# Performance work log

Measured on AMD Instinct MI355X. Metric: run time of the kernel, lower is better.

Reference implementation:

```python
import jax, jax.numpy as jnp
import numpy as np

B, S, D, K = 8, 2048, 1024, 256
LN_EPS = 1e-5


def _freq_positions(input_dim, num_freq, spec_len):
    # torch.linspace(0, input_dim//2, num_freq).long(), clamped to rfft length
    pos = np.linspace(0.0, input_dim // 2, num_freq).astype(np.int64)
    return np.clip(pos, 0, spec_len - 1)


def setup_inputs() -> dict:
    key = jax.random.key(0)
    k1, k2, k3 = jax.random.split(key, 3)
    x = jax.random.normal(k1, (B, S, D), dtype=jnp.float32)
    # magnitude init: init_magnitude=0.1 (small jitter keeps gradients non-degenerate)
    magnitude = 0.1 + 0.01 * jax.random.normal(k2, (K, D), dtype=jnp.float32)
    phase = 0.1 * jax.random.normal(k3, (K, D), dtype=jnp.float32)
    interference_w = 0.01 * jax.random.normal(jax.random.fold_in(key, 7), (K, K), dtype=jnp.float32)
    ln_gamma = jnp.ones((D,), dtype=jnp.float32)
    ln_beta = jnp.zeros((D,), dtype=jnp.float32)
    return {"x": x, "magnitude": magnitude, "phase": phase,
            "interference_w": interference_w, "ln_gamma": ln_gamma, "ln_beta": ln_beta}


def reference(x, magnitude, phase, interference_w, ln_gamma, ln_beta):
    b, s, d = x.shape
    residual = x
    padded_len = 1 << int(np.ceil(np.log2(s)))  # static
    if padded_len > s:
        x = jnp.pad(x, ((0, 0), (0, padded_len - s), (0, 0)))
    # FFT along sequence axis: (B, padded_len//2+1, D) complex
    x_fft = jnp.fft.rfft(x, axis=1)
    freq_pos = _freq_positions(d, magnitude.shape[0], x_fft.shape[1])  # (K,) static ints

    # gather selected frequencies: (B, K, D)
    x_selected = x_fft[:, freq_pos, :]
    # complex weights from magnitude/phase
    cw = (magnitude * jnp.cos(phase) + 1j * magnitude * jnp.sin(phase)).astype(jnp.complex64)
    x_weighted = x_selected * cw[None, :, :]
    # interference on real part: bkd,kj->bjd
    interference = jnp.einsum('bkd,kj->bjd', jnp.real(x_weighted), interference_w)
    x_processed = x_weighted + 0.1 * interference.astype(jnp.complex64)

    # scatter back (positions are unique for these dims)
    x_fft_processed = x_fft.at[:, freq_pos, :].set(x_processed)
    x_rec = jnp.fft.irfft(x_fft_processed, n=padded_len, axis=1)[:, :s, :]

    # residual + LayerNorm over last dim (dropout is identity in eval)
    y = x_rec + residual
    mu = jnp.mean(y, axis=-1, keepdims=True)
    var = jnp.mean(jnp.square(y - mu), axis=-1, keepdims=True)
    y = (y - mu) * jax.lax.rsqrt(var + LN_EPS)
    return y * ln_gamma + ln_beta
```

## Files before the change

### kernel.cpp

```cpp
#include <hip/hip_runtime.h>
#include <math.h>

#define NS 2048
#define ND 1024
#define NK 256
#define NB 8

typedef __attribute__((ext_vector_type(8))) short short8;
typedef __attribute__((ext_vector_type(4))) float f32x4;
typedef __attribute__((ext_vector_type(4))) unsigned short u16x4;
typedef __attribute__((ext_vector_type(8))) unsigned short u16x8;
typedef unsigned int u32;

__device__ __forceinline__ unsigned short f2bf(float x) {
  unsigned int u = __float_as_uint(x);
  u = (u + 0x7fffu + ((u >> 16) & 1u)) >> 16;
  return (unsigned short)u;
}
__device__ __forceinline__ float bf2f(unsigned short h) {
  return __uint_as_float(((unsigned int)h) << 16);
}

__device__ __forceinline__ int fpos(int k) {
  return (k == 255) ? 512 : (int)((float)k * (512.0f / 255.0f));
}

__device__ __forceinline__ void gll16(const unsigned short* g, unsigned short* l) {
  __builtin_amdgcn_global_load_lds(
      (__attribute__((address_space(1))) void*)(void*)const_cast<unsigned short*>(g),
      (__attribute__((address_space(3))) void*)l, 16, 0, 0);
}

__global__ __launch_bounds__(256) void k_master(float* __restrict__ master) {
  int t = blockIdx.x * 256 + threadIdx.x;
  double th = (double)t * (6.283185307179586476925286766559 / 2048.0);
  master[t] = (float)cos(th);
}

__global__ __launch_bounds__(256) void k_tabs(const float* __restrict__ master,
                                              unsigned short* __restrict__ CFi,
                                              unsigned short* __restrict__ CSi) {
  int gid = blockIdx.x * 256 + threadIdx.x;
  if (gid < 512 * 2048) {
    int r = gid >> 11, s = gid & 2047;
    int p = (fpos(r >> 1) * s) & 2047;
    float v = (r & 1) ? -master[(p + 1536) & 2047] : master[p];
    CFi[gid] = f2bf(v);
  } else {
    int g = gid - 512 * 2048;
    int s = g >> 9, c = g & 511;
    int p = (fpos(c >> 1) * s) & 2047;
    float v = (c & 1) ? -master[(p + 1536) & 2047] : master[p];
    CSi[g] = f2bf(v);
  }
}

__global__ __launch_bounds__(256) void k_cw2(const float* __restrict__ mag,
                                             const float* __restrict__ ph,
                                             float* __restrict__ mc,
                                             float* __restrict__ ms,
                                             float* __restrict__ mcT,
                                             float* __restrict__ msT) {
  int bid = blockIdx.x;
  int kt = bid >> 4, dt = bid & 15;
  int t = threadIdx.x;
  __shared__ float lc[64][68], ls[64][68];
  int kl = t >> 4, d4 = (t & 15) * 4;
#pragma unroll
  for (int i = 0; i < 4; i++) {
    int k = i * 16 + kl;
    size_t off = (size_t)(kt * 64 + k) * ND + dt * 64 + d4;
    float4 mg = *(const float4*)&mag[off];
    float4 pp = *(const float4*)&ph[off];
    float m[4] = {mg.x, mg.y, mg.z, mg.w}, p[4] = {pp.x, pp.y, pp.z, pp.w};
    float oc[4], os[4];
#pragma unroll
    for (int q = 0; q < 4; q++) {
      float sp, cp;
      sincosf(p[q], &sp, &cp);
      oc[q] = m[q] * cp;
      os[q] = m[q] * sp;
      lc[k][d4 + q] = oc[q];
      ls[k][d4 + q] = os[q];
    }
    *(float4*)&mc[off] = make_float4(oc[0], oc[1], oc[2], oc[3]);
    *(float4*)&ms[off] = make_float4(os[0], os[1], os[2], os[3]);
  }
  __syncthreads();
  int dl = t >> 2, kc = (t & 3) * 16;
#pragma unroll
  for (int i = 0; i < 16; i += 4) {
    float4 vc = {lc[kc + i][dl], lc[kc + i + 1][dl], lc[kc + i + 2][dl], lc[kc + i + 3][dl]};
    float4 vs = {ls[kc + i][dl], ls[kc + i + 1][dl], ls[kc + i + 2][dl], ls[kc + i + 3][dl]};
    size_t o = (size_t)(dt * 64 + dl) * 256 + kt * 64 + kc + i;
    *(float4*)&mcT[o] = vc;
    *(float4*)&msT[o] = vs;
  }
}

__global__ __launch_bounds__(256) void k_wt(const float* __restrict__ W,
                                            unsigned short* __restrict__ WT) {
  int bid = blockIdx.x;
  int kt = bid >> 2, jt = bid & 3;
  int t = threadIdx.x;
  __shared__ float lw[64][68];
  int kl = t >> 4, j4 = (t & 15) * 4;
#pragma unroll
  for (int i = 0; i < 4; i++) {
    int k = i * 16 + kl;
    float4 wv = *(const float4*)&W[(size_t)(kt * 64 + k) * 256 + jt * 64 + j4];
    lw[k][j4 + 0] = wv.x; lw[k][j4 + 1] = wv.y;
    lw[k][j4 + 2] = wv.z; lw[k][j4 + 3] = wv.w;
  }
  __syncthreads();
  int jl = t >> 2, kc = (t & 3) * 16;
#pragma unroll
  for (int i = 0; i < 16; i += 4) {
    u16x4 v = {f2bf(lw[kc + i][jl]), f2bf(lw[kc + i + 1][jl]),
               f2bf(lw[kc + i + 2][jl]), f2bf(lw[kc + i + 3][jl])};
    *(u16x4*)&WT[(size_t)(jt * 64 + jl) * 256 + kt * 64 + kc + i] = v;
  }
}

__global__ __launch_bounds__(256) void k_conv(const float* __restrict__ x,
                                              unsigned short* __restrict__ xt) {
  int bid = blockIdx.x;
  int b = bid >> 9, rem = bid & 511;
  int s0 = (rem >> 4) * 64, d0 = (rem & 15) * 64;
  int t = threadIdx.x;
  __shared__ __attribute__((aligned(16))) unsigned short lt[64 * 72];
#pragma unroll
  for (int c = 0; c < 4; c++) {
    int e = c * 256 + t;
    int row = e >> 4, col = (e & 15) * 4;
    float4 v = *(const float4*)&x[((size_t)b * NS + s0 + row) * ND + d0 + col];
    lt[(col + 0) * 72 + row] = f2bf(v.x);
    lt[(col + 1) * 72 + row] = f2bf(v.y);
    lt[(col + 2) * 72 + row] = f2bf(v.z);
    lt[(col + 3) * 72 + row] = f2bf(v.w);
  }
  __syncthreads();
  int dl = t >> 2, sc = (t & 3) * 16;
  u16x8 a = *(u16x8*)&lt[dl * 72 + sc];
  u16x8 bb = *(u16x8*)&lt[dl * 72 + sc + 8];
  size_t o = ((size_t)b * ND + d0 + dl) * NS + s0 + sc;
  *(u16x8*)&xt[o] = a;
  *(u16x8*)&xt[o + 8] = bb;
}

template <int BM, int BN, int EPI>
__global__ __launch_bounds__(256) void gemm_db(const unsigned short* __restrict__ A,
                                               const unsigned short* __restrict__ B,
                                               unsigned short* __restrict__ C0,
                                               unsigned short* __restrict__ C1,
                                               const float* __restrict__ P0,
                                               const float* __restrict__ P1,
                                               int M, int N, int K,
                                               size_t sA, size_t sB) {
  constexpr int MI = BM / 32, NI = BN / 32;
  constexpr int NSTG = (BM + BN) / 32;
  const int mt = M / BM, nt = N / BN;
  int nwg = gridDim.x;
  int bid0 = blockIdx.x;
  int bid = (bid0 & 7) * (nwg >> 3) + (bid0 >> 3);
  int b = bid / (mt * nt), r = bid % (mt * nt);
  int m0 = (r / nt) * BM, n0 = (r % nt) * BN;
  int t = threadIdx.x, lane = t & 63, w = t >> 6;
  int wr = (t >> 7) & 1, wc = (t >> 6) & 1;
  __shared__ __attribute__((aligned(16))) unsigned short As[2][BM * 64];
  __shared__ __attribute__((aligned(16))) unsigned short Bs[2][BN * 64];
  const unsigned short* Ag = A + b * sA + (size_t)m0 * K;
  const unsigned short* Bg = B + b * sB + (size_t)n0 * K;
  int arow = lane >> 3;
  int aswz = ((lane & 7) ^ (lane >> 3)) * 8;

  f32x4 acc[MI][NI];
#pragma unroll
  for (int i = 0; i < MI; i++)
#pragma unroll
    for (int j = 0; j < NI; j++) acc[i][j] = {0.f, 0.f, 0.f, 0.f};

  const int nkt = K / 64;

#define STAGE(buf, kt_)                                                       \
  do {                                                                        \
    int kofs = (kt_) * 64;                                                    \
    _Pragma("unroll") for (int i = 0; i < BM / 32; i++) {                     \
      int r0 = w * (BM / 4) + i * 8;                                          \
      gll16(Ag + (size_t)(r0 + arow) * K + kofs + aswz, &As[buf][r0 * 64]);   \
    }                                                                         \
    _Pragma("unroll") for (int i = 0; i < BN / 32; i++) {                     \
      int r0 = w * (BN / 4) + i * 8;                                          \
      gll16(Bg + (size_t)(r0 + arow) * K + kofs + aswz, &Bs[buf][r0 * 64]);   \
    }                                                                         \
  } while (0)

  STAGE(0, 0);
  if (nkt > 1) STAGE(1, 1);

  for (int kt = 0; kt < nkt; kt++) {
    int cur = kt & 1;
    if (kt + 1 < nkt)
      asm volatile("s_waitcnt vmcnt(%0)" ::"n"(NSTG) : "memory");
    else
      asm volatile("s_waitcnt vmcnt(0)" ::: "memory");
    __builtin_amdgcn_s_barrier();
#pragma unroll
    for (int ks = 0; ks < 2; ks++) {
      short8 af[MI], bfv[NI];
#pragma unroll
      for (int mi = 0; mi < MI; mi++) {
        int row = wr * (BM / 2) + mi * 16 + (lane & 15);
        int sl = (ks * 4 + (lane >> 4)) ^ (row & 7);
        af[mi] = *(const short8*)&As[cur][row * 64 + sl * 8];
      }
#pragma unroll
      for (int ni = 0; ni < NI; ni++) {
        int row = wc * (BN / 2) + ni * 16 + (lane & 15);
        int sl = (ks * 4 + (lane >> 4)) ^ (row & 7);
        bfv[ni] = *(const short8*)&Bs[cur][row * 64 + sl * 8];
      }
#pragma unroll
      for (int mi = 0; mi < MI; mi++)
#pragma unroll
        for (int ni = 0; ni < NI; ni++)
          acc[mi][ni] = __builtin_amdgcn_mfma_f32_16x16x32_bf16(
              af[mi], bfv[ni], acc[mi][ni], 0, 0, 0);
    }
    __builtin_amdgcn_s_barrier();
    if (kt + 2 < nkt) STAGE(cur, kt + 2);
  }
#undef STAGE

#pragma unroll
  for (int mi = 0; mi < MI; mi++) {
#pragma unroll
    for (int ni = 0; ni < NI; ni++) {
      int row0 = m0 + wr * (BM / 2) + mi * 16 + ((lane >> 4) * 4);
      int col = n0 + wc * (BN / 2) + ni * 16 + (lane & 15);
      f32x4 a = acc[mi][ni];
      if (EPI == 0) {
#pragma unroll
        for (int q = 0; q < 4; q++)
          C0[((size_t)b * M + row0 + q) * N + col] = f2bf(a[q]);
      } else if (EPI == 1) {
        u16x4 xv = {f2bf(a[0]), f2bf(a[1]), f2bf(a[2]), f2bf(a[3])};
        *(u16x4*)&C0[((size_t)b * N + col) * M + row0] = xv;
        int j0 = row0 >> 1, j1 = j0 + 1;
        float rw0 = P0[(size_t)j0 * ND + col] * a[0] - P1[(size_t)j0 * ND + col] * a[1];
        float rw1 = P0[(size_t)j1 * ND + col] * a[2] - P1[(size_t)j1 * ND + col] * a[3];
        u32 pk = (u32)f2bf(rw0) | ((u32)f2bf(rw1) << 16);
        *(u32*)&C1[((size_t)b * N + col) * (M / 2) + j0] = pk;
      } else {
        float alpha = ((col == 0) ? 1.0f : 2.0f) * (1.0f / 2048.0f);
#pragma unroll
        for (int q = 0; q < 4; q++) {
          int dd = row0 + q;
          u32 reim = *(const u32*)&C1[((size_t)b * M + dd) * 512 + 2 * col];
          float xr = bf2f((unsigned short)(reim & 0xffffu));
          float xi = bf2f((unsigned short)(reim >> 16));
          float mcv = P0[(size_t)dd * 256 + col];
          float msv = P1[(size_t)dd * 256 + col];
          float m1 = mcv - 1.0f;
          float dre = alpha * (m1 * xr - msv * xi + 0.1f * a[q]);
          float dim = alpha * (msv * xr + m1 * xi);
          u32 pk = (u32)f2bf(dre) | ((u32)f2bf(dim) << 16);
          *(u32*)&C0[((size_t)b * M + dd) * 512 + 2 * col] = pk;
        }
      }
    }
  }
}

__global__ __launch_bounds__(256) void k4_ln(const float* __restrict__ x,
                                             const unsigned short* __restrict__ corr,
                                             const float* __restrict__ g,
                                             const float* __restrict__ be,
                                             float* __restrict__ out) {
  int row = blockIdx.x;
  int t = threadIdx.x;
  size_t base = (size_t)row * ND + t * 4;
  u16x4 cv = *(const u16x4*)&corr[base];
  float4 xv = *(const float4*)&x[base];
  float v[4] = {fmaf(2.f, xv.x, bf2f(cv[0])), fmaf(2.f, xv.y, bf2f(cv[1])),
                fmaf(2.f, xv.z, bf2f(cv[2])), fmaf(2.f, xv.w, bf2f(cv[3]))};
  float s = v[0] + v[1] + v[2] + v[3];
  float q = v[0] * v[0] + v[1] * v[1] + v[2] * v[2] + v[3] * v[3];
#pragma unroll
  for (int o = 32; o >= 1; o >>= 1) {
    s += __shfl_xor(s, o, 64);
    q += __shfl_xor(q, o, 64);
  }
  __shared__ float ss[4], qs[4];
  if ((t & 63) == 0) { ss[t >> 6] = s; qs[t >> 6] = q; }
  __syncthreads();
  s = ss[0] + ss[1] + ss[2] + ss[3];
  q = qs[0] + qs[1] + qs[2] + qs[3];
  float mu = s * (1.0f / (float)ND);
  float var = q * (1.0f / (float)ND) - mu * mu;
  float rstd = rsqrtf(var + 1e-5f);
  float4 gv = *(const float4*)&g[t * 4];
  float4 bv = *(const float4*)&be[t * 4];
  float4 ov;
  ov.x = (v[0] - mu) * rstd * gv.x + bv.x;
  ov.y = (v[1] - mu) * rstd * gv.y + bv.y;
  ov.z = (v[2] - mu) * rstd * gv.z + bv.z;
  ov.w = (v[3] - mu) * rstd * gv.w + bv.w;
  *(float4*)&out[base] = ov;
}

extern "C" void kernel_launch(void* const* d_in, const int* in_sizes, int n_in,
                              void* d_out, int out_size, void* d_ws, size_t ws_size,
                              hipStream_t stream) {
  const float* x   = (const float*)d_in[0];
  const float* mag = (const float*)d_in[1];
  const float* ph  = (const float*)d_in[2];
  const float* W   = (const float*)d_in[3];
  const float* g   = (const float*)d_in[4];
  const float* be  = (const float*)d_in[5];
  float* out = (float*)d_out;
  char* w = (char*)d_ws;

  float*          master = (float*)(w);
  unsigned short* CFi    = (unsigned short*)(w + (1ull << 20));
  unsigned short* CSi    = (unsigned short*)(w + (3ull << 20));
  float*          mc     = (float*)(w + (5ull << 20));
  float*          ms     = (float*)(w + (6ull << 20));
  float*          mcT    = (float*)(w + (7ull << 20));
  float*          msT    = (float*)(w + (8ull << 20));
  unsigned short* WT     = (unsigned short*)(w + (9ull << 20));
  unsigned short* XqT    = (unsigned short*)(w + (10ull << 20));
  unsigned short* RXwT   = (unsigned short*)(w + (18ull << 20));
  unsigned short* DltT   = (unsigned short*)(w + (22ull << 20));
  unsigned short* corr   = (unsigned short*)(w + (30ull << 20));
  unsigned short* xt     = (unsigned short*)(w + (62ull << 20));

  k_master<<<8, 256, 0, stream>>>(master);
  k_tabs<<<8192, 256, 0, stream>>>(master, CFi, CSi);
  k_cw2<<<64, 256, 0, stream>>>(mag, ph, mc, ms, mcT, msT);
  k_wt<<<16, 256, 0, stream>>>(W, WT);
  k_conv<<<4096, 256, 0, stream>>>(x, xt);
  gemm_db<128, 64, 1><<<512, 256, 0, stream>>>(CFi, xt, XqT, RXwT, mc, ms,
                                               512, 1024, 2048, 0,
                                               (size_t)1024 * 2048);
  gemm_db<128, 64, 2><<<256, 256, 0, stream>>>(RXwT, WT, DltT, XqT, mcT, msT,
                                               1024, 256, 256,
                                               (size_t)1024 * 256, 0);
  gemm_db<128, 128, 0><<<1024, 256, 0, stream>>>(CSi, DltT, corr, nullptr,
                                                 nullptr, nullptr,
                                                 2048, 1024, 512, 0,
                                                 (size_t)1024 * 512);
  k4_ln<<<16384, 256, 0, stream>>>(x, corr, g, be, out);
}
```

Before: 225.3 us.

## Fuse prep kernels, load GEMM A operand from global, triple-buffer B, row-per-wave LN

Merges the master-cosine, table, complex-weight, weight-transpose and x-transpose kernels into one launch, and computes the twiddles with sincosf directly instead of through a lookup table. The GEMM now reads the A operand straight from global memory into registers and keeps only B in LDS with three buffers. This halves LDS use and moves the next-stage prefetch ahead of the MFMAs, but the A loads are uncoalesced and unswizzled. The LayerNorm kernel gives one row to each wave, which removes the shared-memory reduction and the block sync.

```diff
diff --git a/kernel.cpp b/kernel.cpp
--- a/kernel.cpp
+++ b/kernel.cpp
@@ -31,125 +31,120 @@
       (__attribute__((address_space(3))) void*)l, 16, 0, 0);
 }
 
-__global__ __launch_bounds__(256) void k_master(float* __restrict__ master) {
-  int t = blockIdx.x * 256 + threadIdx.x;
-  double th = (double)t * (6.283185307179586476925286766559 / 2048.0);
-  master[t] = (float)cos(th);
-}
-
-__global__ __launch_bounds__(256) void k_tabs(const float* __restrict__ master,
+__global__ __launch_bounds__(256) void k_prep(const float* __restrict__ mag,
+                                              const float* __restrict__ ph,
+                                              const float* __restrict__ W,
+                                              const float* __restrict__ x,
                                               unsigned short* __restrict__ CFi,
-                                              unsigned short* __restrict__ CSi) {
-  int gid = blockIdx.x * 256 + threadIdx.x;
-  if (gid < 512 * 2048) {
-    int r = gid >> 11, s = gid & 2047;
-    int p = (fpos(r >> 1) * s) & 2047;
-    float v = (r & 1) ? -master[(p + 1536) & 2047] : master[p];
-    CFi[gid] = f2bf(v);
+                                              unsigned short* __restrict__ CSi,
+                                              float* __restrict__ mc,
+                                              float* __restrict__ ms,
+                                              float* __restrict__ mcT,
+                                              float* __restrict__ msT,
+                                              unsigned short* __restrict__ WT,
+                                              unsigned short* __restrict__ xt) {
+  __shared__ __attribute__((aligned(16))) char smem[34816];
+  int bid = blockIdx.x, t = threadIdx.x;
+  const float C2PI = 0.0030679615757712823f;
+  if (bid < 8192) {
+    int gid = bid * 256 + t;
+    if (gid < 512 * 2048) {
+      int r = gid >> 11, s = gid & 2047;
+      int p = (fpos(r >> 1) * s) & 2047;
+      float sn, cs;
+      sincosf((float)p * C2PI, &sn, &cs);
+      CFi[gid] = f2bf((r & 1) ? -sn : cs);
+    } else {
+      int g2 = gid - 512 * 2048;
+      int s = g2 >> 9, c = g2 & 511;
+      int p = (fpos(c >> 1) * s) & 2047;
+      float sn, cs;
+      sincosf((float)p * C2PI, &sn, &cs);
+      CSi[g2] = f2bf((c & 1) ? -sn : cs);
+    }
+  } else if (bid < 8256) {
+    int lb = bid - 8192;
+    int kt = lb >> 4, dt = lb & 15;
+    float(*lc)[68] = (float(*)[68])smem;
+    float(*ls)[68] = (float(*)[68])(smem + 17408);
+    int kl = t >> 4, d4 = (t & 15) * 4;
+#pragma unroll
+    for (int i = 0; i < 4; i++) {
+      int k = i * 16 + kl;
+      size_t off = (size_t)(kt * 64 + k) * ND + dt * 64 + d4;
+      float4 mg = *(const float4*)&mag[off];
+      float4 pp = *(const float4*)&ph[off];
+      float m[4] = {mg.x, mg.y, mg.z, mg.w}, p[4] = {pp.x, pp.y, pp.z, pp.w};
+      float oc[4], os[4];
+#pragma unroll
+      for (int q = 0; q < 4; q++) {
+        float sp, cp;
+        sincosf(p[q], &sp, &cp);
+        oc[q] = m[q] * cp;
+        os[q] = m[q] * sp;
+        lc[k][d4 + q] = oc[q];
+        ls[k][d4 + q] = os[q];
+      }
+      *(float4*)&mc[off] = make_float4(oc[0], oc[1], oc[2], oc[3]);
+      *(float4*)&ms[off] = make_float4(os[0], os[1], os[2], os[3]);
+    }
+    __syncthreads();
+    int dl = t >> 2, kc = (t & 3) * 16;
+#pragma unroll
+    for (int i = 0; i < 16; i += 4) {
+      float4 vc = {lc[kc + i][dl], lc[kc + i + 1][dl], lc[kc + i + 2][dl], lc[kc + i + 3][dl]};
+      float4 vs = {ls[kc + i][dl], ls[kc + i + 1][dl], ls[kc + i + 2][dl], ls[kc + i + 3][dl]};
+      size_t o = (size_t)(dt * 64 + dl) * 256 + kt * 64 + kc + i;
+      *(float4*)&mcT[o] = vc;
+      *(float4*)&msT[o] = vs;
+    }
+  } else if (bid < 8272) {
+    int lb = bid - 8256;
+    int kt = lb >> 2, jt = lb & 3;
+    float(*lw)[68] = (float(*)[68])smem;
+    int kl = t >> 4, j4 = (t & 15) * 4;
+#pragma unroll
+    for (int i = 0; i < 4; i++) {
+      int k = i * 16 + kl;
+      float4 wv = *(const float4*)&W[(size_t)(kt * 64 + k) * 256 + jt * 64 + j4];
+      lw[k][j4 + 0] = wv.x; lw[k][j4 + 1] = wv.y;
+      lw[k][j4 + 2] = wv.z; lw[k][j4 + 3] = wv.w;
+    }
+    __syncthreads();
+    int jl = t >> 2, kc = (t & 3) * 16;
+#pragma unroll
+    for (int i = 0; i < 16; i += 4) {
+      u16x4 v = {f2bf(lw[kc + i][jl]), f2bf(lw[kc + i + 1][jl]),
+                 f2bf(lw[kc + i + 2][jl]), f2bf(lw[kc + i + 3][jl])};
+      *(u16x4*)&WT[(size_t)(jt * 64 + jl) * 256 + kt * 64 + kc + i] = v;
+    }
   } else {
-    int g = gid - 512 * 2048;
-    int s = g >> 9, c = g & 511;
-    int p = (fpos(c >> 1) * s) & 2047;
-    float v = (c & 1) ? -master[(p + 1536) & 2047] : master[p];
-    CSi[g] = f2bf(v);
-  }
-}
-
-__global__ __launch_bounds__(256) void k_cw2(const float* __restrict__ mag,
-                                             const float* __restrict__ ph,
-                                             float* __restrict__ mc,
-                                             float* __restrict__ ms,
-                                             float* __restrict__ mcT,
-                                             float* __restrict__ msT) {
-  int bid = blockIdx.x;
-  int kt = bid >> 4, dt = bid & 15;
-  int t = threadIdx.x;
-  __shared__ float lc[64][68], ls[64][68];
-  int kl = t >> 4, d4 = (t & 15) * 4;
-#pragma unroll
-  for (int i = 0; i < 4; i++) {
-    int k = i * 16 + kl;
-    size_t off = (size_t)(kt * 64 + k) * ND + dt * 64 + d4;
-    float4 mg = *(const float4*)&mag[off];
-    float4 pp = *(const float4*)&ph[off];
-    float m[4] = {mg.x, mg.y, mg.z, mg.w}, p[4] = {pp.x, pp.y, pp.z, pp.w};
-    float oc[4], os[4];
-#pragma unroll
-    for (int q = 0; q < 4; q++) {
-      float sp, cp;
-      sincosf(p[q], &sp, &cp);
-      oc[q] = m[q] * cp;
-      os[q] = m[q] * sp;
-      lc[k][d4 + q] = oc[q];
-      ls[k][d4 + q] = os[q];
-    }
-    *(float4*)&mc[off] = make_float4(oc[0], oc[1], oc[2], oc[3]);
-    *(float4*)&ms[off] = make_float4(os[0], os[1], os[2], os[3]);
-  }
-  __syncthreads();
-  int dl = t >> 2, kc = (t & 3) * 16;
-#pragma unroll
-  for (int i = 0; i < 16; i += 4) {
-    float4 vc = {lc[kc + i][dl], lc[kc + i + 1][dl], lc[kc + i + 2][dl], lc[kc + i + 3][dl]};
-    float4 vs = {ls[kc + i][dl], ls[kc + i + 1][dl], ls[kc + i + 2][dl], ls[kc + i + 3][dl]};
-    size_t o = (size_t)(dt * 64 + dl) * 256 + kt * 64 + kc + i;
-    *(float4*)&mcT[o] = vc;
-    *(float4*)&msT[o] = vs;
-  }
-}
-
-__global__ __launch_bounds__(256) void k_wt(const float* __restrict__ W,
-                                            unsigned short* __restrict__ WT) {
-  int bid = blockIdx.x;
-  int kt = bid >> 2, jt = bid & 3;
-  int t = threadIdx.x;
-  __shared__ float lw[64][68];
-  int kl = t >> 4, j4 = (t & 15) * 4;
-#pragma unroll
-  for (int i = 0; i < 4; i++) {
-    int k = i * 16 + kl;
-    float4 wv = *(const float4*)&W[(size_t)(kt * 64 + k) * 256 + jt * 64 + j4];
-    lw[k][j4 + 0] = wv.x; lw[k][j4 + 1] = wv.y;
-    lw[k][j4 + 2] = wv.z; lw[k][j4 + 3] = wv.w;
-  }
-  __syncthreads();
-  int jl = t >> 2, kc = (t & 3) * 16;
-#pragma unroll
-  for (int i = 0; i < 16; i += 4) {
-    u16x4 v = {f2bf(lw[kc + i][jl]), f2bf(lw[kc + i + 1][jl]),
-               f2bf(lw[kc + i + 2][jl]), f2bf(lw[kc + i + 3][jl])};
-    *(u16x4*)&WT[(size_t)(jt * 64 + jl) * 256 + kt * 64 + kc + i] = v;
-  }
-}
-
-__global__ __launch_bounds__(256) void k_conv(const float* __restrict__ x,
-                                              unsigned short* __restrict__ xt) {
-  int bid = blockIdx.x;
-  int b = bid >> 9, rem = bid & 511;
-  int s0 = (rem >> 4) * 64, d0 = (rem & 15) * 64;
-  int t = threadIdx.x;
-  __shared__ __attribute__((aligned(16))) unsigned short lt[64 * 72];
-#pragma unroll
-  for (int c = 0; c < 4; c++) {
-    int e = c * 256 + t;
-    int row = e >> 4, col = (e & 15) * 4;
-    float4 v = *(const float4*)&x[((size_t)b * NS + s0 + row) * ND + d0 + col];
-    lt[(col + 0) * 72 + row] = f2bf(v.x);
-    lt[(col + 1) * 72 + row] = f2bf(v.y);
-    lt[(col + 2) * 72 + row] = f2bf(v.z);
-    lt[(col + 3) * 72 + row] = f2bf(v.w);
-  }
-  __syncthreads();
-  int dl = t >> 2, sc = (t & 3) * 16;
-  u16x8 a = *(u16x8*)&lt[dl * 72 + sc];
-  u16x8 bb = *(u16x8*)&lt[dl * 72 + sc + 8];
-  size_t o = ((size_t)b * ND + d0 + dl) * NS + s0 + sc;
-  *(u16x8*)&xt[o] = a;
-  *(u16x8*)&xt[o + 8] = bb;
+    int lb = bid - 8272;
+    int b = lb >> 9, rem = lb & 511;
+    int s0 = (rem >> 4) * 64, d0 = (rem & 15) * 64;
+    unsigned short* lt = (unsigned short*)smem;
+#pragma unroll
+    for (int c = 0; c < 4; c++) {
+      int e = c * 256 + t;
+      int row = e >> 4, col = (e & 15) * 4;
+      float4 v = *(const float4*)&x[((size_t)b * NS + s0 + row) * ND + d0 + col];
+      lt[(col + 0) * 72 + row] = f2bf(v.x);
+      lt[(col + 1) * 72 + row] = f2bf(v.y);
+      lt[(col + 2) * 72 + row] = f2bf(v.z);
+      lt[(col + 3) * 72 + row] = f2bf(v.w);
+    }
+    __syncthreads();
+    int dl = t >> 2, sc = (t & 3) * 16;
+    u16x8 a = *(u16x8*)&lt[dl * 72 + sc];
+    u16x8 bb = *(u16x8*)&lt[dl * 72 + sc + 8];
+    size_t o = ((size_t)b * ND + d0 + dl) * NS + s0 + sc;
+    *(u16x8*)&xt[o] = a;
+    *(u16x8*)&xt[o + 8] = bb;
+  }
 }
 
 template <int BM, int BN, int EPI>
-__global__ __launch_bounds__(256) void gemm_db(const unsigned short* __restrict__ A,
+__global__ __launch_bounds__(256) void gemm_rs(const unsigned short* __restrict__ A,
                                                const unsigned short* __restrict__ B,
                                                unsigned short* __restrict__ C0,
                                                unsigned short* __restrict__ C1,
@@ -158,7 +153,7 @@
                                                int M, int N, int K,
                                                size_t sA, size_t sB) {
   constexpr int MI = BM / 32, NI = BN / 32;
-  constexpr int NSTG = (BM + BN) / 32;
+  constexpr int NSTG_B = BN / 32;
   const int mt = M / BM, nt = N / BN;
   int nwg = gridDim.x;
   int bid0 = blockIdx.x;
@@ -167,8 +162,7 @@
   int m0 = (r / nt) * BM, n0 = (r % nt) * BN;
   int t = threadIdx.x, lane = t & 63, w = t >> 6;
   int wr = (t >> 7) & 1, wc = (t >> 6) & 1;
-  __shared__ __attribute__((aligned(16))) unsigned short As[2][BM * 64];
-  __shared__ __attribute__((aligned(16))) unsigned short Bs[2][BN * 64];
+  __shared__ __attribute__((aligned(16))) unsigned short Bs[3 * BN * 64];
   const unsigned short* Ag = A + b * sA + (size_t)m0 * K;
   const unsigned short* Bg = B + b * sB + (size_t)n0 * K;
   int arow = lane >> 3;
@@ -182,55 +176,57 @@
 
   const int nkt = K / 64;
 
-#define STAGE(buf, kt_)                                                       \
+#define STAGE_B(buf, kt_)                                                     \
   do {                                                                        \
     int kofs = (kt_) * 64;                                                    \
-    _Pragma("unroll") for (int i = 0; i < BM / 32; i++) {                     \
-      int r0 = w * (BM / 4) + i * 8;                                          \
-      gll16(Ag + (size_t)(r0 + arow) * K + kofs + aswz, &As[buf][r0 * 64]);   \
-    }                                                                         \
     _Pragma("unroll") for (int i = 0; i < BN / 32; i++) {                     \
       int r0 = w * (BN / 4) + i * 8;                                          \
-      gll16(Bg + (size_t)(r0 + arow) * K + kofs + aswz, &Bs[buf][r0 * 64]);   \
+      gll16(Bg + (size_t)(r0 + arow) * K + kofs + aswz,                       \
+            &Bs[(buf) * (BN * 64) + r0 * 64]);                                \
     }                                                                         \
   } while (0)
 
-  STAGE(0, 0);
-  if (nkt > 1) STAGE(1, 1);
+  STAGE_B(0, 0);
+  if (nkt > 1) STAGE_B(1, 1);
 
   for (int kt = 0; kt < nkt; kt++) {
-    int cur = kt & 1;
+    int cur = kt % 3;
     if (kt + 1 < nkt)
-      asm volatile("s_waitcnt vmcnt(%0)" ::"n"(NSTG) : "memory");
+      asm volatile("s_waitcnt vmcnt(%0)" ::"n"(NSTG_B) : "memory");
     else
       asm volatile("s_waitcnt vmcnt(0)" ::: "memory");
     __builtin_amdgcn_s_barrier();
-#pragma unroll
-    for (int ks = 0; ks < 2; ks++) {
-      short8 af[MI], bfv[NI];
+    short8 av[2][MI];
+#pragma unroll
+    for (int ks = 0; ks < 2; ks++)
 #pragma unroll
       for (int mi = 0; mi < MI; mi++) {
         int row = wr * (BM / 2) + mi * 16 + (lane & 15);
-        int sl = (ks * 4 + (lane >> 4)) ^ (row & 7);
-        af[mi] = *(const short8*)&As[cur][row * 64 + sl * 8];
+        av[ks][mi] = *(const short8*)&Ag[(size_t)row * K + kt * 64 + ks * 32 +
+                                         (lane >> 4) * 8];
       }
+    short8 bfv[2][NI];
+#pragma unroll
+    for (int ks = 0; ks < 2; ks++)
 #pragma unroll
       for (int ni = 0; ni < NI; ni++) {
         int row = wc * (BN / 2) + ni * 16 + (lane & 15);
         int sl = (ks * 4 + (lane >> 4)) ^ (row & 7);
-        bfv[ni] = *(const short8*)&Bs[cur][row * 64 + sl * 8];
+        bfv[ks][ni] = *(const short8*)&Bs[cur * (BN * 64) + row * 64 + sl * 8];
       }
+    __builtin_amdgcn_sched_barrier(0);
+    if (kt + 2 < nkt) STAGE_B((kt + 2) % 3, kt + 2);
+#pragma unroll
+    for (int ks = 0; ks < 2; ks++)
 #pragma unroll
       for (int mi = 0; mi < MI; mi++)
 #pragma unroll
         for (int ni = 0; ni < NI; ni++)
           acc[mi][ni] = __builtin_amdgcn_mfma_f32_16x16x32_bf16(
-              af[mi], bfv[ni], acc[mi][ni], 0, 0, 0);
-    }
+              av[ks][mi], bfv[ks][ni], acc[mi][ni], 0, 0, 0);
     __builtin_amdgcn_s_barrier();
-    if (kt + 2 < nkt) STAGE(cur, kt + 2);
-  }
-#undef STAGE
+  }
+#undef STAGE_B
 
 #pragma unroll
   for (int mi = 0; mi < MI; mi++) {
@@ -277,36 +273,45 @@
                                              const float* __restrict__ g,
                                              const float* __restrict__ be,
                                              float* __restrict__ out) {
-  int row = blockIdx.x;
-  int t = threadIdx.x;
-  size_t base = (size_t)row * ND + t * 4;
-  u16x4 cv = *(const u16x4*)&corr[base];
-  float4 xv = *(const float4*)&x[base];
-  float v[4] = {fmaf(2.f, xv.x, bf2f(cv[0])), fmaf(2.f, xv.y, bf2f(cv[1])),
-                fmaf(2.f, xv.z, bf2f(cv[2])), fmaf(2.f, xv.w, bf2f(cv[3]))};
-  float s = v[0] + v[1] + v[2] + v[3];
-  float q = v[0] * v[0] + v[1] * v[1] + v[2] * v[2] + v[3] * v[3];
+  int lane = threadIdx.x & 63;
+  int row = blockIdx.x * 4 + (threadIdx.x >> 6);
+  size_t base = (size_t)row * ND + lane * 16;
+  u16x8 c0 = *(const u16x8*)&corr[base];
+  u16x8 c1 = *(const u16x8*)&corr[base + 8];
+  float v[16];
+#pragma unroll
+  for (int i = 0; i < 4; i++) {
+    float4 xv = *(const float4*)&x[base + i * 4];
+    float xx[4] = {xv.x, xv.y, xv.z, xv.w};
+#pragma unroll
+    for (int q = 0; q < 4; q++) {
+      int e = i * 4 + q;
+      float cr = bf2f(e < 8 ? c0[e & 7] : c1[e & 7]);
+      v[e] = fmaf(2.f, xx[q], cr);
+    }
+  }
+  float s = 0.f, qq = 0.f;
+#pragma unroll
+  for (int e = 0; e < 16; e++) { s += v[e]; qq += v[e] * v[e]; }
 #pragma unroll
   for (int o = 32; o >= 1; o >>= 1) {
     s += __shfl_xor(s, o, 64);
-    q += __shfl_xor(q, o, 64);
-  }
-  __shared__ float ss[4], qs[4];
-  if ((t & 63) == 0) { ss[t >> 6] = s; qs[t >> 6] = q; }
-  __syncthreads();
-  s = ss[0] + ss[1] + ss[2] + ss[3];
-  q = qs[0] + qs[1] + qs[2] + qs[3];
+    qq += __shfl_xor(qq, o, 64);
+  }
   float mu = s * (1.0f / (float)ND);
-  float var = q * (1.0f / (float)ND) - mu * mu;
+  float var = qq * (1.0f / (float)ND) - mu * mu;
   float rstd = rsqrtf(var + 1e-5f);
-  float4 gv = *(const float4*)&g[t * 4];
-  float4 bv = *(const float4*)&be[t * 4];
-  float4 ov;
-  ov.x = (v[0] - mu) * rstd * gv.x + bv.x;
-  ov.y = (v[1] - mu) * rstd * gv.y + bv.y;
-  ov.z = (v[2] - mu) * rstd * gv.z + bv.z;
-  ov.w = (v[3] - mu) * rstd * gv.w + bv.w;
-  *(float4*)&out[base] = ov;
+#pragma unroll
+  for (int i = 0; i < 4; i++) {
+    float4 gv = *(const float4*)&g[lane * 16 + i * 4];
+    float4 bv = *(const float4*)&be[lane * 16 + i * 4];
+    float4 ov;
+    ov.x = (v[i * 4 + 0] - mu) * rstd * gv.x + bv.x;
+    ov.y = (v[i * 4 + 1] - mu) * rstd * gv.y + bv.y;
+    ov.z = (v[i * 4 + 2] - mu) * rstd * gv.z + bv.z;
+    ov.w = (v[i * 4 + 3] - mu) * rstd * gv.w + bv.w;
+    *(float4*)&out[base + i * 4] = ov;
+  }
 }
 
 extern "C" void kernel_launch(void* const* d_in, const int* in_sizes, int n_in,
@@ -321,34 +326,29 @@
   float* out = (float*)d_out;
   char* w = (char*)d_ws;
 
-  float*          master = (float*)(w);
-  unsigned short* CFi    = (unsigned short*)(w + (1ull << 20));
-  unsigned short* CSi    = (unsigned short*)(w + (3ull << 20));
-  float*          mc     = (float*)(w + (5ull << 20));
-  float*          ms     = (float*)(w + (6ull << 20));
-  float*          mcT    = (float*)(w + (7ull << 20));
-  float*          msT    = (float*)(w + (8ull << 20));
-  unsigned short* WT     = (unsigned short*)(w + (9ull << 20));
-  unsigned short* XqT    = (unsigned short*)(w + (10ull << 20));
-  unsigned short* RXwT   = (unsigned short*)(w + (18ull << 20));
-  unsigned short* DltT   = (unsigned short*)(w + (22ull << 20));
-  unsigned short* corr   = (unsigned short*)(w + (30ull << 20));
-  unsigned short* xt     = (unsigned short*)(w + (62ull << 20));
-
-  k_master<<<8, 256, 0, stream>>>(master);
-  k_tabs<<<8192, 256, 0, stream>>>(master, CFi, CSi);
-  k_cw2<<<64, 256, 0, stream>>>(mag, ph, mc, ms, mcT, msT);
-  k_wt<<<16, 256, 0, stream>>>(W, WT);
-  k_conv<<<4096, 256, 0, stream>>>(x, xt);
-  gemm_db<128, 64, 1><<<512, 256, 0, stream>>>(CFi, xt, XqT, RXwT, mc, ms,
+  unsigned short* CFi  = (unsigned short*)(w);
+  unsigned short* CSi  = (unsigned short*)(w + (2ull << 20));
+  float*          mc   = (float*)(w + (4ull << 20));
+  float*          ms   = (float*)(w + (5ull << 20));
+  float*          mcT  = (float*)(w + (6ull << 20));
+  float*          msT  = (float*)(w + (7ull << 20));
+  unsigned short* WT   = (unsigned short*)(w + (8ull << 20));
+  unsigned short* XqT  = (unsigned short*)(w + (9ull << 20));
+  unsigned short* RXwT = (unsigned short*)(w + (17ull << 20));
+  unsigned short* DltT = (unsigned short*)(w + (21ull << 20));
+  unsigned short* corr = (unsigned short*)(w + (29ull << 20));
+  unsigned short* xt   = (unsigned short*)(w + (61ull << 20));
+
+  k_prep<<<12368, 256, 0, stream>>>(mag, ph, W, x, CFi, CSi, mc, ms, mcT, msT, WT, xt);
+  gemm_rs<128, 64, 1><<<512, 256, 0, stream>>>(CFi, xt, XqT, RXwT, mc, ms,
                                                512, 1024, 2048, 0,
                                                (size_t)1024 * 2048);
-  gemm_db<128, 64, 2><<<256, 256, 0, stream>>>(RXwT, WT, DltT, XqT, mcT, msT,
+  gemm_rs<128, 64, 2><<<256, 256, 0, stream>>>(RXwT, WT, DltT, XqT, mcT, msT,
                                                1024, 256, 256,
                                                (size_t)1024 * 256, 0);
-  gemm_db<128, 128, 0><<<1024, 256, 0, stream>>>(CSi, DltT, corr, nullptr,
+  gemm_rs<128, 128, 0><<<1024, 256, 0, stream>>>(CSi, DltT, corr, nullptr,
                                                  nullptr, nullptr,
                                                  2048, 1024, 512, 0,
                                                  (size_t)1024 * 512);
-  k4_ln<<<16384, 256, 0, stream>>>(x, corr, g, be, out);
-}
+  k4_ln<<<4096, 256, 0, stream>>>(x, corr, g, be, out);
+}
```

New measurement: 274.7 us. +21.9%, slower.
